# Kernel optimization log

Hardware: AMD Instinct MI355X
Metric: run time of the kernel (lower is better)

## Reference

```python
import jax, jax.numpy as jnp
import numpy as np

N_NODES = 50000
N_EDGES = 800000
N_GRAPHS = 64
IN_CH = 128
HID = [64, 128]
MLP_CH = [128, 64, 64, 64, 1]


def _glorot(key, fan_in, fan_out):
    lim = jnp.sqrt(6.0 / (fan_in + fan_out))
    return jax.random.uniform(key, (fan_in, fan_out), jnp.float32, -lim, lim)


def setup_inputs() -> dict:
    key = jax.random.key(0)
    ks = jax.random.split(key, 16)
    x = jax.random.normal(ks[0], (N_NODES, IN_CH), jnp.float32)
    edge_index = jax.random.randint(ks[1], (2, N_EDGES), 0, N_NODES, jnp.int64)
    batch = jnp.sort(jax.random.randint(ks[2], (N_NODES,), 0, N_GRAPHS, jnp.int64))
    inp = {"x": x, "edge_index": edge_index, "batch": batch}
    # GCNConv weights (x @ W + b)
    inp["W1"] = _glorot(ks[3], IN_CH, HID[0]);  inp["b1"] = jnp.zeros((HID[0],), jnp.float32)
    inp["W2"] = _glorot(ks[4], HID[0], HID[1]); inp["b2"] = jnp.zeros((HID[1],), jnp.float32)
    # MLP weights
    for i in range(4):
        inp[f"M{i+1}"] = _glorot(ks[5 + i], MLP_CH[i], MLP_CH[i + 1])
        inp[f"c{i+1}"] = jnp.zeros((MLP_CH[i + 1],), jnp.float32)
    return inp


def _gcn_conv(x, src, dst, dinv, W, b):
    # x' = D^-1/2 (A + I) D^-1/2 (x W) + b, via gather-scale-scatter over edges
    h = x @ W                                   # [N, F]
    norm = dinv[src] * dinv[dst]                # [E+N]
    msg = h[src] * norm[:, None]                # gather + scale
    out = jax.ops.segment_sum(msg, dst, num_segments=x.shape[0])
    return out + b


def reference(x, edge_index, batch, W1, b1, W2, b2, M1, c1, M2, c2, M3, c3, M4, c4):
    N = x.shape[0]
    x = x.astype(jnp.float32)
    # add self loops (PyG GCNConv default)
    loops = jnp.arange(N, dtype=edge_index.dtype)
    src = jnp.concatenate([edge_index[0], loops])
    dst = jnp.concatenate([edge_index[1], loops])
    deg = jax.ops.segment_sum(jnp.ones_like(src, jnp.float32), dst, num_segments=N)
    dinv = jnp.where(deg > 0, jax.lax.rsqrt(jnp.maximum(deg, 1.0)), 0.0)

    h = jax.nn.relu(_gcn_conv(x, src, dst, dinv, W1, b1))
    h = jax.nn.relu(_gcn_conv(h, src, dst, dinv, W2, b2))

    # global mean pool per graph
    sums = jax.ops.segment_sum(h, batch, num_segments=N_GRAPHS)
    cnts = jax.ops.segment_sum(jnp.ones((N,), jnp.float32), batch, num_segments=N_GRAPHS)
    g = sums / jnp.maximum(cnts, 1.0)[:, None]   # [G, 128]

    # MLP (eval mode: dropout is identity)
    g = jax.nn.leaky_relu(g @ M1 + c1, negative_slope=0.2)
    g = jax.nn.leaky_relu(g @ M2 + c2, negative_slope=0.1)
    g = jax.nn.leaky_relu(g @ M3 + c3, negative_slope=0.1)
    g = jax.nn.relu(g @ M4 + c4)
    return g
```

## Files before the change

### kernel.cpp

```cpp
#include <hip/hip_runtime.h>
#include <hip/hip_fp16.h>

#define N_NODES 50000
#define N_EDGES 800000
#define N_GRAPHS 64

#define SCAN_BLOCK 256
#define SCAN_ITEMS 4
#define SCAN_CHUNK (SCAN_BLOCK * SCAN_ITEMS)
#define NB_SCAN ((N_NODES + SCAN_CHUNK - 1) / SCAN_CHUNK)

#define FILL_STRIPES 256

struct __align__(8) h4v { __half2 a, b; };


__global__ void k_zero(int* __restrict__ deg, float* __restrict__ sums) {
    int i = blockIdx.x * 256 + threadIdx.x;
    if (i < N_NODES) deg[i] = 0;
    if (i < N_GRAPHS * 128) sums[i] = 0.f;
}


__global__ void k_deg_part(const int* __restrict__ dst, int* __restrict__ deg, int E) {
    const int range = blockIdx.x & 7;
    const int stripe = blockIdx.x >> 3;
    const int lo = range * (N_NODES / 8);
    const int hi = lo + (N_NODES / 8);
    for (int e = stripe * 256 + threadIdx.x; e < E; e += FILL_STRIPES * 256) {
        int d = dst[e];
        if (d >= lo && d < hi) atomicAdd(&deg[d], 1);
    }
}

__global__ void k_scan1(const int* __restrict__ deg, int* __restrict__ part) {
    __shared__ int lds[SCAN_BLOCK];
    int b = blockIdx.x, t = threadIdx.x;
    int base = b * SCAN_CHUNK + t * SCAN_ITEMS;
    int s = 0;
#pragma unroll
    for (int k = 0; k < SCAN_ITEMS; ++k) {
        int i = base + k;
        if (i < N_NODES) s += deg[i];
    }
    lds[t] = s;
    __syncthreads();
    for (int off = SCAN_BLOCK / 2; off > 0; off >>= 1) {
        if (t < off) lds[t] += lds[t + off];
        __syncthreads();
    }
    if (t == 0) part[b] = lds[0];
}

__global__ void k_scan3(const int* __restrict__ deg, const int* __restrict__ part,
                        int* __restrict__ row_ptr, int* __restrict__ fill,
                        float* __restrict__ dinv) {
    __shared__ int lds[SCAN_BLOCK];
    __shared__ int pl[64];
    __shared__ int basePfx;
    int b = blockIdx.x, t = threadIdx.x;
    if (t < NB_SCAN) pl[t] = part[t];
    int base = b * SCAN_CHUNK + t * SCAN_ITEMS;
    int v[SCAN_ITEMS];
    int s = 0;
#pragma unroll
    for (int k = 0; k < SCAN_ITEMS; ++k) {
        int i = base + k;
        v[k] = (i < N_NODES) ? deg[i] : 0;
        s += v[k];
    }
    lds[t] = s;
    __syncthreads();
    if (t == 0) {
        int acc = 0;
        for (int i = 0; i < b; ++i) acc += pl[i];
        basePfx = acc;
    }
    for (int off = 1; off < SCAN_BLOCK; off <<= 1) {
        int val = (t >= off) ? lds[t - off] : 0;
        __syncthreads();
        lds[t] += val;
        __syncthreads();
    }
    int excl = (t == 0 ? 0 : lds[t - 1]) + basePfx;
#pragma unroll
    for (int k = 0; k < SCAN_ITEMS; ++k) {
        int i = base + k;
        if (i < N_NODES) {
            row_ptr[i] = excl;
            fill[i] = excl;
            dinv[i] = rsqrtf((float)(v[k] + 1));
            excl += v[k];
            if (i == N_NODES - 1) row_ptr[N_NODES] = excl;
        }
    }
}

__global__ void k_fill_part(const int* __restrict__ src, const int* __restrict__ dst,
                            int* __restrict__ fill, unsigned short* __restrict__ csr, int E) {
    const int range = blockIdx.x & 7;
    const int stripe = blockIdx.x >> 3;
    const int lo = range * (N_NODES / 8);
    const int hi = lo + (N_NODES / 8);
    for (int e = stripe * 256 + threadIdx.x; e < E; e += FILL_STRIPES * 256) {
        int d = dst[e];
        if (d >= lo && d < hi) {
            int pos = atomicAdd(&fill[d], 1);
            csr[pos] = (unsigned short)src[e];
        }
    }
}


__global__ __launch_bounds__(256) void k_gemm1(const float* __restrict__ A,
                                               const float* __restrict__ W,
                                               const float* __restrict__ dscale,
                                               __half* __restrict__ Cout, int N) {
    const int FIN = 128;
    __shared__ __align__(16) float As[64 * (FIN + 2)];
    __shared__ __align__(16) float Wsm[FIN * 64];
    const int t = threadIdx.x;
    const int row0 = blockIdx.x * 64;

    const int NF4 = 64 * FIN / 4;
    for (int idx = t; idx < NF4; idx += 256) {
        int r = idx / (FIN / 4);
        int c4 = idx % (FIN / 4);
        float4 v = make_float4(0.f, 0.f, 0.f, 0.f);
        if (row0 + r < N) v = ((const float4*)(A + (size_t)(row0 + r) * FIN))[c4];
        float* p = &As[r * (FIN + 2) + c4 * 4];
        ((float2*)p)[0] = make_float2(v.x, v.y);
        ((float2*)p)[1] = make_float2(v.z, v.w);
    }
    for (int idx = t; idx < FIN * 16; idx += 256) {
        int r = idx / 16, c4 = idx % 16;
        *((float4*)&Wsm[r * 64 + c4 * 4]) = ((const float4*)(W + (size_t)r * 64))[c4];
    }
    __syncthreads();

    const int tc = (t & 15) * 4;
    const int tr = (t >> 4) * 4;
    float acc[4][4] = {};
#pragma unroll 4
    for (int k = 0; k < FIN; k += 2) {
        float2 a[4];
#pragma unroll
        for (int r = 0; r < 4; ++r)
            a[r] = *(const float2*)&As[(tr + r) * (FIN + 2) + k];
        float4 w0 = *(const float4*)&Wsm[k * 64 + tc];
        float4 w1 = *(const float4*)&Wsm[(k + 1) * 64 + tc];
#pragma unroll
        for (int r = 0; r < 4; ++r) {
            acc[r][0] = fmaf(a[r].x, w0.x, acc[r][0]);
            acc[r][1] = fmaf(a[r].x, w0.y, acc[r][1]);
            acc[r][2] = fmaf(a[r].x, w0.z, acc[r][2]);
            acc[r][3] = fmaf(a[r].x, w0.w, acc[r][3]);
            acc[r][0] = fmaf(a[r].y, w1.x, acc[r][0]);
            acc[r][1] = fmaf(a[r].y, w1.y, acc[r][1]);
            acc[r][2] = fmaf(a[r].y, w1.z, acc[r][2]);
            acc[r][3] = fmaf(a[r].y, w1.w, acc[r][3]);
        }
    }

#pragma unroll
    for (int r = 0; r < 4; ++r) {
        int row = row0 + tr + r;
        if (row < N) {
            float s = dscale[row];
            __half2* dsth = (__half2*)(Cout + (size_t)row * 64 + tc);
            dsth[0] = __floats2half2_rn(acc[r][0] * s, acc[r][1] * s);
            dsth[1] = __floats2half2_rn(acc[r][2] * s, acc[r][3] * s);
        }
    }
}


template <bool RELU>
__global__ void k_agg(const h4v* __restrict__ h, const float* __restrict__ dinv,
                      const int* __restrict__ row_ptr, const unsigned short* __restrict__ csr,
                      const float* __restrict__ bias, h4v* __restrict__ out, int N) {
    int node = blockIdx.x * 16 + (threadIdx.x >> 4);
    int lane = threadIdx.x & 15;
    if (node >= N) return;
    float di = dinv[node];
    h4v sv = h[(size_t)node * 16 + lane];
    float2 pa = __half22float2(sv.a), pb = __half22float2(sv.b);
    float x0 = pa.x, y0 = pa.y, z0 = pb.x, w0 = pb.y;
    float x1 = 0, y1 = 0, z1 = 0, w1 = 0;
    float x2 = 0, y2 = 0, z2 = 0, w2 = 0;
    float x3 = 0, y3 = 0, z3 = 0, w3 = 0;
    int beg = row_ptr[node], end = row_ptr[node + 1];
    int j = beg;
    for (; j + 4 <= end; j += 4) {
        int s0 = csr[j], s1 = csr[j + 1], s2 = csr[j + 2], s3 = csr[j + 3];
        h4v v0 = h[(size_t)s0 * 16 + lane];
        h4v v1 = h[(size_t)s1 * 16 + lane];
        h4v v2 = h[(size_t)s2 * 16 + lane];
        h4v v3 = h[(size_t)s3 * 16 + lane];
        float2 a0 = __half22float2(v0.a), b0 = __half22float2(v0.b);
        float2 a1 = __half22float2(v1.a), b1 = __half22float2(v1.b);
        float2 a2 = __half22float2(v2.a), b2 = __half22float2(v2.b);
        float2 a3 = __half22float2(v3.a), b3 = __half22float2(v3.b);
        x0 += a0.x; y0 += a0.y; z0 += b0.x; w0 += b0.y;
        x1 += a1.x; y1 += a1.y; z1 += b1.x; w1 += b1.y;
        x2 += a2.x; y2 += a2.y; z2 += b2.x; w2 += b2.y;
        x3 += a3.x; y3 += a3.y; z3 += b3.x; w3 += b3.y;
    }
    for (; j < end; ++j) {
        h4v v = h[(size_t)csr[j] * 16 + lane];
        float2 a = __half22float2(v.a), b = __half22float2(v.b);
        x0 += a.x; y0 += a.y; z0 += b.x; w0 += b.y;
    }
    float sx = (x0 + x1) + (x2 + x3);
    float sy = (y0 + y1) + (y2 + y3);
    float sz = (z0 + z1) + (z2 + z3);
    float sw = (w0 + w1) + (w2 + w3);
    h4v o;
    if (RELU) {
        float4 bv = ((const float4*)bias)[lane];
        float vx = fmaf(sx, di, bv.x); vx = vx > 0.f ? vx : 0.f;
        float vy = fmaf(sy, di, bv.y); vy = vy > 0.f ? vy : 0.f;
        float vz = fmaf(sz, di, bv.z); vz = vz > 0.f ? vz : 0.f;
        float vw = fmaf(sw, di, bv.w); vw = vw > 0.f ? vw : 0.f;
        o.a = __floats2half2_rn(di * vx, di * vy);
        o.b = __floats2half2_rn(di * vz, di * vw);
    } else {
        o.a = __floats2half2_rn(sx * di, sy * di);
        o.b = __floats2half2_rn(sz * di, sw * di);
    }
    out[(size_t)node * 16 + lane] = o;
}


__global__ __launch_bounds__(256) void k_gemm_pool(const __half2* __restrict__ A2,
                                                   const float* __restrict__ W,
                                                   const float* __restrict__ bias,
                                                   const int* __restrict__ batch,
                                                   float* __restrict__ sums, int N) {
    __shared__ __align__(16) float As[64 * 66];
    __shared__ __align__(16) float Wsm[64 * 64];
    __shared__ float red[16][68];
    __shared__ int batchLDS[64];
    const int t = threadIdx.x;
    const int row0 = blockIdx.x * 64;
    const int coff = blockIdx.y * 64;

    for (int idx = t; idx < 64 * 32; idx += 256) {
        int r = idx >> 5, c2 = idx & 31;
        float2 v = make_float2(0.f, 0.f);
        if (row0 + r < N) v = __half22float2(A2[(size_t)(row0 + r) * 32 + c2]);
        *(float2*)&As[r * 66 + c2 * 2] = v;
    }
    for (int idx = t; idx < 64 * 16; idx += 256) {
        int r = idx >> 4, c4 = idx & 15;
        *(float4*)&Wsm[r * 64 + c4 * 4] = *(const float4*)&W[(size_t)r * 128 + coff + c4 * 4];
    }
    if (t < 64) batchLDS[t] = batch[min(row0 + t, N - 1)];
    __syncthreads();

    const int tc = (t & 15) * 4;
    const int tr = (t >> 4) * 4;
    float acc[4][4] = {};
#pragma unroll 4
    for (int k = 0; k < 64; k += 2) {
        float2 a[4];
#pragma unroll
        for (int r = 0; r < 4; ++r)
            a[r] = *(const float2*)&As[(tr + r) * 66 + k];
        float4 w0 = *(const float4*)&Wsm[k * 64 + tc];
        float4 w1 = *(const float4*)&Wsm[(k + 1) * 64 + tc];
#pragma unroll
        for (int r = 0; r < 4; ++r) {
            acc[r][0] = fmaf(a[r].x, w0.x, acc[r][0]);
            acc[r][1] = fmaf(a[r].x, w0.y, acc[r][1]);
            acc[r][2] = fmaf(a[r].x, w0.z, acc[r][2]);
            acc[r][3] = fmaf(a[r].x, w0.w, acc[r][3]);
            acc[r][0] = fmaf(a[r].y, w1.x, acc[r][0]);
            acc[r][1] = fmaf(a[r].y, w1.y, acc[r][1]);
            acc[r][2] = fmaf(a[r].y, w1.z, acc[r][2]);
            acc[r][3] = fmaf(a[r].y, w1.w, acc[r][3]);
        }
    }

    float4 bv = *(const float4*)&bias[coff + tc];
    float v[4][4];
#pragma unroll
    for (int r = 0; r < 4; ++r) {
        bool valid = (row0 + tr + r) < N;
        v[r][0] = valid ? fmaxf(acc[r][0] + bv.x, 0.f) : 0.f;
        v[r][1] = valid ? fmaxf(acc[r][1] + bv.y, 0.f) : 0.f;
        v[r][2] = valid ? fmaxf(acc[r][2] + bv.z, 0.f) : 0.f;
        v[r][3] = valid ? fmaxf(acc[r][3] + bv.w, 0.f) : 0.f;
    }

    const int g0 = batchLDS[0], g1 = batchLDS[63];
    const int trg = t >> 4;
    for (int g = g0; g <= g1; ++g) {
        float p0 = 0.f, p1 = 0.f, p2 = 0.f, p3 = 0.f;
#pragma unroll
        for (int r = 0; r < 4; ++r) {
            if (batchLDS[tr + r] == g) { p0 += v[r][0]; p1 += v[r][1]; p2 += v[r][2]; p3 += v[r][3]; }
        }
        red[trg][tc + 0] = p0; red[trg][tc + 1] = p1;
        red[trg][tc + 2] = p2; red[trg][tc + 3] = p3;
        __syncthreads();
        for (int off = 8; off > 0; off >>= 1) {
            if (trg < off) {
#pragma unroll
                for (int c = 0; c < 4; ++c) red[trg][tc + c] += red[trg + off][tc + c];
            }
            __syncthreads();
        }
        if (t < 16) {
#pragma unroll
            for (int c = 0; c < 4; ++c)
                atomicAdd(&sums[g * 128 + coff + t * 4 + c], red[0][t * 4 + c]);
        }
        __syncthreads();
    }
}


__global__ void k_mlp(const float* __restrict__ sums, const int* __restrict__ batch, int N,
                      const float* __restrict__ M1, const float* __restrict__ c1,
                      const float* __restrict__ M2, const float* __restrict__ c2,
                      const float* __restrict__ M3, const float* __restrict__ c3,
                      const float* __restrict__ M4, const float* __restrict__ c4,
                      float* __restrict__ out) {
    __shared__ float g[128], t1[64], t2[64], t3[64];
    __shared__ float cntb;
    int b = blockIdx.x;
    int t = threadIdx.x;
    if (t == 0) {
        int lo = 0, hi = N;
        while (lo < hi) { int m = (lo + hi) >> 1; if (batch[m] < b) lo = m + 1; else hi = m; }
        int lb = lo;
        lo = 0; hi = N;
        while (lo < hi) { int m = (lo + hi) >> 1; if (batch[m] <= b) lo = m + 1; else hi = m; }
        cntb = fmaxf((float)(lo - lb), 1.0f);
    }
    __syncthreads();
    if (t < 128) g[t] = sums[b * 128 + t] / cntb;
    __syncthreads();
    if (t < 64) {
        float acc = c1[t];
        for (int k = 0; k < 128; ++k) acc = fmaf(g[k], M1[k * 64 + t], acc);
        t1[t] = acc >= 0.f ? acc : 0.2f * acc;
    }
    __syncthreads();
    if (t < 64) {
        float acc = c2[t];
        for (int k = 0; k < 64; ++k) acc = fmaf(t1[k], M2[k * 64 + t], acc);
        t2[t] = acc >= 0.f ? acc : 0.1f * acc;
    }
    __syncthreads();
    if (t < 64) {
        float acc = c3[t];
        for (int k = 0; k < 64; ++k) acc = fmaf(t2[k], M3[k * 64 + t], acc);
        t3[t] = acc >= 0.f ? acc : 0.1f * acc;
    }
    __syncthreads();
    if (t == 0) {
        float acc = c4[0];
        for (int k = 0; k < 64; ++k) acc = fmaf(t3[k], M4[k], acc);
        out[b] = fmaxf(acc, 0.f);
    }
}


extern "C" void kernel_launch(void* const* d_in, const int* in_sizes, int n_in,
                              void* d_out, int out_size, void* d_ws, size_t ws_size,
                              hipStream_t stream) {
    const float* x   = (const float*)d_in[0];
    const int*   ei  = (const int*)d_in[1];
    const int*   bat = (const int*)d_in[2];
    const float* W1  = (const float*)d_in[3];
    const float* b1  = (const float*)d_in[4];
    const float* W2  = (const float*)d_in[5];
    const float* b2  = (const float*)d_in[6];
    const float* M1  = (const float*)d_in[7];
    const float* c1  = (const float*)d_in[8];
    const float* M2  = (const float*)d_in[9];
    const float* c2  = (const float*)d_in[10];
    const float* M3  = (const float*)d_in[11];
    const float* c3  = (const float*)d_in[12];
    const float* M4  = (const float*)d_in[13];
    const float* c4  = (const float*)d_in[14];
    float* out = (float*)d_out;

    const int* src = ei;
    const int* dst = ei + N_EDGES;

    float* bufA    = (float*)d_ws;
    float* bufB    = bufA + (size_t)N_NODES * 64;
    float* dinv    = bufB + (size_t)N_NODES * 64;
    float* sums    = dinv + N_NODES;
    int*   deg     = (int*)(sums + N_GRAPHS * 128);
    int*   row_ptr = deg + N_NODES;
    int*   fill    = row_ptr + N_NODES + 1;
    int*   part    = fill + N_NODES;
    unsigned short* csr = (unsigned short*)(part + 64);

    k_zero<<<(N_NODES + 255) / 256, 256, 0, stream>>>(deg, sums);
    k_deg_part<<<8 * FILL_STRIPES, 256, 0, stream>>>(dst, deg, N_EDGES);
    k_scan1<<<NB_SCAN, SCAN_BLOCK, 0, stream>>>(deg, part);
    k_scan3<<<NB_SCAN, SCAN_BLOCK, 0, stream>>>(deg, part, row_ptr, fill, dinv);
    k_fill_part<<<8 * FILL_STRIPES, 256, 0, stream>>>(src, dst, fill, csr, N_EDGES);

    const int NBLK = (N_NODES + 63) / 64;
    const int ABLK = (N_NODES + 15) / 16;

    k_gemm1<<<NBLK, 256, 0, stream>>>(x, W1, dinv, (__half*)bufA, N_NODES);
    k_agg<true><<<ABLK, 256, 0, stream>>>(
        (const h4v*)bufA, dinv, row_ptr, csr, b1, (h4v*)bufB, N_NODES);

    k_agg<false><<<ABLK, 256, 0, stream>>>(
        (const h4v*)bufB, dinv, row_ptr, csr, nullptr, (h4v*)bufA, N_NODES);
    k_gemm_pool<<<dim3(NBLK, 2), 256, 0, stream>>>(
        (const __half2*)bufA, W2, b2, bat, sums, N_NODES);

    k_mlp<<<N_GRAPHS, 128, 0, stream>>>(sums, bat, N_NODES,
                                        M1, c1, M2, c2, M3, c3, M4, c4, out);
}
```

Measured before the change: 263.7 us.

## Fuse second aggregation with GEMM+pool, pack edges, fuse scan kernels

Merges the second-layer aggregation into the GEMM+mean-pool kernel, so aggregated features go straight into LDS and are never written to and re-read from global memory. Each block now computes all 128 output columns instead of splitting them over two y-blocks. Edges are packed into a single 32-bit word (dst<<16|src) so the degree and fill passes read one array instead of two. The two scan kernels become one, with each block recomputing its prefix from the raw degrees, which saves a launch at the cost of redundant reads. W2 is converted to fp16, which adds some rounding error, and the fused kernel has a longer dependent gather phase before its GEMM.

```diff
diff --git a/kernel.cpp b/kernel.cpp
--- a/kernel.cpp
+++ b/kernel.cpp
@@ -15,51 +15,51 @@
 struct __align__(8) h4v { __half2 a, b; };
 
 
-__global__ void k_zero(int* __restrict__ deg, float* __restrict__ sums) {
+__global__ void k_zero_pack(int* __restrict__ deg, float* __restrict__ sums,
+                            const int* __restrict__ src, const int* __restrict__ dst,
+                            unsigned* __restrict__ pk,
+                            const float* __restrict__ W2, __half* __restrict__ w2h) {
     int i = blockIdx.x * 256 + threadIdx.x;
     if (i < N_NODES) deg[i] = 0;
     if (i < N_GRAPHS * 128) sums[i] = 0.f;
-}
-
-
-__global__ void k_deg_part(const int* __restrict__ dst, int* __restrict__ deg, int E) {
+    if (i < 64 * 128) w2h[i] = __float2half_rn(W2[i]);
+    if (i < N_EDGES) pk[i] = ((unsigned)dst[i] << 16) | (unsigned)src[i];
+}
+
+
+__global__ void k_deg_part(const unsigned* __restrict__ pk, int* __restrict__ deg, int E) {
     const int range = blockIdx.x & 7;
     const int stripe = blockIdx.x >> 3;
-    const int lo = range * (N_NODES / 8);
-    const int hi = lo + (N_NODES / 8);
+    const unsigned lo = range * (N_NODES / 8);
+    const unsigned hi = lo + (N_NODES / 8);
     for (int e = stripe * 256 + threadIdx.x; e < E; e += FILL_STRIPES * 256) {
-        int d = dst[e];
+        unsigned d = pk[e] >> 16;
         if (d >= lo && d < hi) atomicAdd(&deg[d], 1);
     }
 }
 
-__global__ void k_scan1(const int* __restrict__ deg, int* __restrict__ part) {
+__global__ void k_scan_fused(const int* __restrict__ deg,
+                             int* __restrict__ row_ptr, int* __restrict__ fill,
+                             float* __restrict__ dinv) {
     __shared__ int lds[SCAN_BLOCK];
+    __shared__ int basePfx;
     int b = blockIdx.x, t = threadIdx.x;
-    int base = b * SCAN_CHUNK + t * SCAN_ITEMS;
-    int s = 0;
-#pragma unroll
-    for (int k = 0; k < SCAN_ITEMS; ++k) {
-        int i = base + k;
-        if (i < N_NODES) s += deg[i];
-    }
-    lds[t] = s;
+    const int4* dg4 = (const int4*)deg;
+
+    int pre = 0;
+    for (int i = t; i < b * 256; i += SCAN_BLOCK) {
+        int4 q = dg4[i];
+        pre += q.x + q.y + q.z + q.w;
+    }
+    lds[t] = pre;
     __syncthreads();
     for (int off = SCAN_BLOCK / 2; off > 0; off >>= 1) {
         if (t < off) lds[t] += lds[t + off];
         __syncthreads();
     }
-    if (t == 0) part[b] = lds[0];
-}
-
-__global__ void k_scan3(const int* __restrict__ deg, const int* __restrict__ part,
-                        int* __restrict__ row_ptr, int* __restrict__ fill,
-                        float* __restrict__ dinv) {
-    __shared__ int lds[SCAN_BLOCK];
-    __shared__ int pl[64];
-    __shared__ int basePfx;
-    int b = blockIdx.x, t = threadIdx.x;
-    if (t < NB_SCAN) pl[t] = part[t];
+    if (t == 0) basePfx = lds[0];
+    __syncthreads();
+
     int base = b * SCAN_CHUNK + t * SCAN_ITEMS;
     int v[SCAN_ITEMS];
     int s = 0;
@@ -71,11 +71,6 @@
     }
     lds[t] = s;
     __syncthreads();
-    if (t == 0) {
-        int acc = 0;
-        for (int i = 0; i < b; ++i) acc += pl[i];
-        basePfx = acc;
-    }
     for (int off = 1; off < SCAN_BLOCK; off <<= 1) {
         int val = (t >= off) ? lds[t - off] : 0;
         __syncthreads();
@@ -96,17 +91,18 @@
     }
 }
 
-__global__ void k_fill_part(const int* __restrict__ src, const int* __restrict__ dst,
-                            int* __restrict__ fill, unsigned short* __restrict__ csr, int E) {
+__global__ void k_fill_part(const unsigned* __restrict__ pk, int* __restrict__ fill,
+                            unsigned short* __restrict__ csr, int E) {
     const int range = blockIdx.x & 7;
     const int stripe = blockIdx.x >> 3;
-    const int lo = range * (N_NODES / 8);
-    const int hi = lo + (N_NODES / 8);
+    const unsigned lo = range * (N_NODES / 8);
+    const unsigned hi = lo + (N_NODES / 8);
     for (int e = stripe * 256 + threadIdx.x; e < E; e += FILL_STRIPES * 256) {
-        int d = dst[e];
+        unsigned p = pk[e];
+        unsigned d = p >> 16;
         if (d >= lo && d < hi) {
             int pos = atomicAdd(&fill[d], 1);
-            csr[pos] = (unsigned short)src[e];
+            csr[pos] = (unsigned short)(p & 0xffffu);
         }
     }
 }
@@ -232,60 +228,100 @@
 }
 
 
-__global__ __launch_bounds__(256) void k_gemm_pool(const __half2* __restrict__ A2,
-                                                   const float* __restrict__ W,
-                                                   const float* __restrict__ bias,
-                                                   const int* __restrict__ batch,
-                                                   float* __restrict__ sums, int N) {
-    __shared__ __align__(16) float As[64 * 66];
-    __shared__ __align__(16) float Wsm[64 * 64];
-    __shared__ float red[16][68];
+#define AS_STRIDE 68
+
+__global__ __launch_bounds__(256) void k_aggemm_pool(
+    const h4v* __restrict__ h, const float* __restrict__ dinv,
+    const int* __restrict__ row_ptr, const unsigned short* __restrict__ csr,
+    const __half2* __restrict__ w2h,
+    const float* __restrict__ bias,
+    const int* __restrict__ batch,
+    float* __restrict__ sums, int N) {
+    __shared__ __align__(16) float As[64 * AS_STRIDE];
+    __shared__ __align__(16) __half2 Wh[64 * 64];
+    __shared__ float red[8][132];
     __shared__ int batchLDS[64];
     const int t = threadIdx.x;
     const int row0 = blockIdx.x * 64;
-    const int coff = blockIdx.y * 64;
-
-    for (int idx = t; idx < 64 * 32; idx += 256) {
-        int r = idx >> 5, c2 = idx & 31;
-        float2 v = make_float2(0.f, 0.f);
-        if (row0 + r < N) v = __half22float2(A2[(size_t)(row0 + r) * 32 + c2]);
-        *(float2*)&As[r * 66 + c2 * 2] = v;
-    }
-    for (int idx = t; idx < 64 * 16; idx += 256) {
-        int r = idx >> 4, c4 = idx & 15;
-        *(float4*)&Wsm[r * 64 + c4 * 4] = *(const float4*)&W[(size_t)r * 128 + coff + c4 * 4];
-    }
+
+    for (int idx = t; idx < 4096; idx += 256) Wh[idx] = w2h[idx];
     if (t < 64) batchLDS[t] = batch[min(row0 + t, N - 1)];
-    __syncthreads();
-
-    const int tc = (t & 15) * 4;
-    const int tr = (t >> 4) * 4;
-    float acc[4][4] = {};
+
+    const int lane = t & 15;
+    const int grp = t >> 4;
+    for (int nn = 0; nn < 4; ++nn) {
+        int node = row0 + nn * 16 + grp;
+        float4 res = make_float4(0.f, 0.f, 0.f, 0.f);
+        if (node < N) {
+            float di = dinv[node];
+            h4v sv = h[(size_t)node * 16 + lane];
+            float2 pa = __half22float2(sv.a), pb = __half22float2(sv.b);
+            float x0 = pa.x, y0 = pa.y, z0 = pb.x, w0 = pb.y;
+            float x1 = 0, y1 = 0, z1 = 0, w1 = 0;
+            float x2 = 0, y2 = 0, z2 = 0, w2 = 0;
+            float x3 = 0, y3 = 0, z3 = 0, w3 = 0;
+            int beg = row_ptr[node], end = row_ptr[node + 1];
+            int j = beg;
+            for (; j + 4 <= end; j += 4) {
+                int s0 = csr[j], s1 = csr[j + 1], s2 = csr[j + 2], s3 = csr[j + 3];
+                h4v v0 = h[(size_t)s0 * 16 + lane];
+                h4v v1 = h[(size_t)s1 * 16 + lane];
+                h4v v2 = h[(size_t)s2 * 16 + lane];
+                h4v v3 = h[(size_t)s3 * 16 + lane];
+                float2 a0 = __half22float2(v0.a), b0 = __half22float2(v0.b);
+                float2 a1 = __half22float2(v1.a), b1 = __half22float2(v1.b);
+                float2 a2 = __half22float2(v2.a), b2 = __half22float2(v2.b);
+                float2 a3 = __half22float2(v3.a), b3 = __half22float2(v3.b);
+                x0 += a0.x; y0 += a0.y; z0 += b0.x; w0 += b0.y;
+                x1 += a1.x; y1 += a1.y; z1 += b1.x; w1 += b1.y;
+                x2 += a2.x; y2 += a2.y; z2 += b2.x; w2 += b2.y;
+                x3 += a3.x; y3 += a3.y; z3 += b3.x; w3 += b3.y;
+            }
+            for (; j < end; ++j) {
+                h4v v = h[(size_t)csr[j] * 16 + lane];
+                float2 a = __half22float2(v.a), b = __half22float2(v.b);
+                x0 += a.x; y0 += a.y; z0 += b.x; w0 += b.y;
+            }
+            float sx = ((x0 + x1) + (x2 + x3)) * di;
+            float sy = ((y0 + y1) + (y2 + y3)) * di;
+            float sz = ((z0 + z1) + (z2 + z3)) * di;
+            float sw = ((w0 + w1) + (w2 + w3)) * di;
+            res = make_float4(sx, sy, sz, sw);
+        }
+        *(float4*)&As[(nn * 16 + grp) * AS_STRIDE + lane * 4] = res;
+    }
+    __syncthreads();
+
+    const int tc = (t & 31) * 4;
+    const int tr = (t >> 5) * 8;
+    float acc[8][4] = {};
 #pragma unroll 4
     for (int k = 0; k < 64; k += 2) {
-        float2 a[4];
-#pragma unroll
-        for (int r = 0; r < 4; ++r)
-            a[r] = *(const float2*)&As[(tr + r) * 66 + k];
-        float4 w0 = *(const float4*)&Wsm[k * 64 + tc];
-        float4 w1 = *(const float4*)&Wsm[(k + 1) * 64 + tc];
-#pragma unroll
-        for (int r = 0; r < 4; ++r) {
-            acc[r][0] = fmaf(a[r].x, w0.x, acc[r][0]);
-            acc[r][1] = fmaf(a[r].x, w0.y, acc[r][1]);
-            acc[r][2] = fmaf(a[r].x, w0.z, acc[r][2]);
-            acc[r][3] = fmaf(a[r].x, w0.w, acc[r][3]);
-            acc[r][0] = fmaf(a[r].y, w1.x, acc[r][0]);
-            acc[r][1] = fmaf(a[r].y, w1.y, acc[r][1]);
-            acc[r][2] = fmaf(a[r].y, w1.z, acc[r][2]);
-            acc[r][3] = fmaf(a[r].y, w1.w, acc[r][3]);
-        }
-    }
-
-    float4 bv = *(const float4*)&bias[coff + tc];
-    float v[4][4];
-#pragma unroll
-    for (int r = 0; r < 4; ++r) {
+        float2 a[8];
+#pragma unroll
+        for (int r = 0; r < 8; ++r)
+            a[r] = *(const float2*)&As[(tr + r) * AS_STRIDE + k];
+        h4v wv0 = *(const h4v*)&Wh[k * 64 + (tc >> 1)];
+        h4v wv1 = *(const h4v*)&Wh[(k + 1) * 64 + (tc >> 1)];
+        float2 w00 = __half22float2(wv0.a), w01 = __half22float2(wv0.b);
+        float2 w10 = __half22float2(wv1.a), w11 = __half22float2(wv1.b);
+#pragma unroll
+        for (int r = 0; r < 8; ++r) {
+            acc[r][0] = fmaf(a[r].x, w00.x, acc[r][0]);
+            acc[r][1] = fmaf(a[r].x, w00.y, acc[r][1]);
+            acc[r][2] = fmaf(a[r].x, w01.x, acc[r][2]);
+            acc[r][3] = fmaf(a[r].x, w01.y, acc[r][3]);
+            acc[r][0] = fmaf(a[r].y, w10.x, acc[r][0]);
+            acc[r][1] = fmaf(a[r].y, w10.y, acc[r][1]);
+            acc[r][2] = fmaf(a[r].y, w11.x, acc[r][2]);
+            acc[r][3] = fmaf(a[r].y, w11.y, acc[r][3]);
+        }
+    }
+
+    float4 bv = *(const float4*)&bias[tc];
+    float v[8][4];
+#pragma unroll
+    for (int r = 0; r < 8; ++r) {
         bool valid = (row0 + tr + r) < N;
         v[r][0] = valid ? fmaxf(acc[r][0] + bv.x, 0.f) : 0.f;
         v[r][1] = valid ? fmaxf(acc[r][1] + bv.y, 0.f) : 0.f;
@@ -294,27 +330,27 @@
     }
 
     const int g0 = batchLDS[0], g1 = batchLDS[63];
-    const int trg = t >> 4;
+    const int rg = t >> 5;
     for (int g = g0; g <= g1; ++g) {
         float p0 = 0.f, p1 = 0.f, p2 = 0.f, p3 = 0.f;
 #pragma unroll
-        for (int r = 0; r < 4; ++r) {
+        for (int r = 0; r < 8; ++r) {
             if (batchLDS[tr + r] == g) { p0 += v[r][0]; p1 += v[r][1]; p2 += v[r][2]; p3 += v[r][3]; }
         }
-        red[trg][tc + 0] = p0; red[trg][tc + 1] = p1;
-        red[trg][tc + 2] = p2; red[trg][tc + 3] = p3;
+        red[rg][tc + 0] = p0; red[rg][tc + 1] = p1;
+        red[rg][tc + 2] = p2; red[rg][tc + 3] = p3;
         __syncthreads();
-        for (int off = 8; off > 0; off >>= 1) {
-            if (trg < off) {
-#pragma unroll
-                for (int c = 0; c < 4; ++c) red[trg][tc + c] += red[trg + off][tc + c];
+        for (int off = 4; off > 0; off >>= 1) {
+            if (rg < off) {
+#pragma unroll
+                for (int c = 0; c < 4; ++c) red[rg][tc + c] += red[rg + off][tc + c];
             }
             __syncthreads();
         }
-        if (t < 16) {
+        if (rg == 0) {
 #pragma unroll
             for (int c = 0; c < 4; ++c)
-                atomicAdd(&sums[g * 128 + coff + t * 4 + c], red[0][t * 4 + c]);
+                atomicAdd(&sums[g * 128 + tc + c], red[0][tc + c]);
         }
         __syncthreads();
     }
@@ -400,12 +436,13 @@
     int*   fill    = row_ptr + N_NODES + 1;
     int*   part    = fill + N_NODES;
     unsigned short* csr = (unsigned short*)(part + 64);
-
-    k_zero<<<(N_NODES + 255) / 256, 256, 0, stream>>>(deg, sums);
-    k_deg_part<<<8 * FILL_STRIPES, 256, 0, stream>>>(dst, deg, N_EDGES);
-    k_scan1<<<NB_SCAN, SCAN_BLOCK, 0, stream>>>(deg, part);
-    k_scan3<<<NB_SCAN, SCAN_BLOCK, 0, stream>>>(deg, part, row_ptr, fill, dinv);
-    k_fill_part<<<8 * FILL_STRIPES, 256, 0, stream>>>(src, dst, fill, csr, N_EDGES);
+    unsigned* pk   = (unsigned*)(csr + N_EDGES);
+    __half* w2h    = (__half*)(pk + N_EDGES);
+
+    k_zero_pack<<<(N_EDGES + 255) / 256, 256, 0, stream>>>(deg, sums, src, dst, pk, W2, w2h);
+    k_deg_part<<<8 * FILL_STRIPES, 256, 0, stream>>>(pk, deg, N_EDGES);
+    k_scan_fused<<<NB_SCAN, SCAN_BLOCK, 0, stream>>>(deg, row_ptr, fill, dinv);
+    k_fill_part<<<8 * FILL_STRIPES, 256, 0, stream>>>(pk, fill, csr, N_EDGES);
 
     const int NBLK = (N_NODES + 63) / 64;
     const int ABLK = (N_NODES + 15) / 16;
@@ -414,10 +451,8 @@
     k_agg<true><<<ABLK, 256, 0, stream>>>(
         (const h4v*)bufA, dinv, row_ptr, csr, b1, (h4v*)bufB, N_NODES);
 
-    k_agg<false><<<ABLK, 256, 0, stream>>>(
-        (const h4v*)bufB, dinv, row_ptr, csr, nullptr, (h4v*)bufA, N_NODES);
-    k_gemm_pool<<<dim3(NBLK, 2), 256, 0, stream>>>(
-        (const __half2*)bufA, W2, b2, bat, sums, N_NODES);
+    k_aggemm_pool<<<NBLK, 256, 0, stream>>>(
+        (const h4v*)bufB, dinv, row_ptr, csr, (const __half2*)w2h, b2, bat, sums, N_NODES);
 
     k_mlp<<<N_GRAPHS, 128, 0, stream>>>(sums, bat, N_NODES,
                                         M1, c1, M2, c2, M3, c3, M4, c4, out);
```

Measured after the change: 286.6 us. 8.7% more time.
